# Optimization experiments

Measured on AMD Instinct MI355X. Metric: run time of the kernel, lower is better.

## Reference

```python
import jax, jax.numpy as jnp
import numpy as np

EPS_FEAT = 1.0 + 1e-4   # feature_map offset: elu(x) + 1.0 + 0.0001
EPS_DEN = 1e-6


def setup_inputs() -> dict:
    key = jax.random.key(0)
    k1, k2, k3 = jax.random.split(key, 3)
    B, L, D = 4, 4096, 1024
    x = jax.random.normal(k1, (B, L, D), dtype=jnp.float32)
    # torch Linear-style init scale ~ 1/sqrt(fan_in)
    W_qkv = jax.random.normal(k2, (D, 3 * D), dtype=jnp.float32) / np.sqrt(D)
    b_qkv = jnp.zeros((3 * D,), dtype=jnp.float32)
    W_out = jax.random.normal(k3, (D, D), dtype=jnp.float32) / np.sqrt(D)
    b_out = jnp.zeros((D,), dtype=jnp.float32)
    return {"x": x, "W_qkv": W_qkv, "b_qkv": b_qkv, "W_out": W_out, "b_out": b_out}


def _linear_attention(x, W_qkv, b_qkv, W_out, b_out, num_heads=16):
    B, L, D = x.shape
    H = num_heads
    E = D // H

    qkv = x @ W_qkv + b_qkv                       # (B, L, 3D)
    q, k, v = jnp.split(qkv, 3, axis=-1)
    q = q.reshape(B, L, H, E)
    k = k.reshape(B, L, H, E)
    v = v.reshape(B, L, H, E)

    q = jax.nn.elu(q * (E ** -0.5)) + EPS_FEAT    # scale BEFORE feature map (as in source)
    k = jax.nn.elu(k) + EPS_FEAT

    # Causal linear attention via recurrence over L; math identical to
    # cumsum of k \otimes v outer products, but never materializes (B,L,H,E,E).
    qL = jnp.moveaxis(q, 1, 0)                    # (L, B, H, E)
    kL = jnp.moveaxis(k, 1, 0)
    vL = jnp.moveaxis(v, 1, 0)

    kv0 = jnp.zeros((B, H, E, E), dtype=x.dtype)
    ks0 = jnp.zeros((B, H, E), dtype=x.dtype)

    def step(carry, qkv_t):
        kv_s, k_s = carry
        q_t, k_t, v_t = qkv_t                     # each (B, H, E)
        kv_s = kv_s + jnp.einsum('bhe,bhf->bhef', k_t, v_t)
        k_s = k_s + k_t
        num = jnp.einsum('bhe,bhef->bhf', q_t, kv_s)           # (B, H, E)
        den = jnp.einsum('bhe,bhe->bh', q_t, k_s)[..., None] + EPS_DEN
        return (kv_s, k_s), num / den

    _, out = jax.lax.scan(step, (kv0, ks0), (qL, kL, vL))       # out: (L, B, H, E)
    out = jnp.moveaxis(out, 0, 1).reshape(B, L, D)
    # dropout is identity in eval mode
    return out @ W_out + b_out


def reference(x, W_qkv, b_qkv, W_out, b_out):
    return _linear_attention(x, W_qkv, b_qkv, W_out, b_out)
```

## Files before the change

### kernel.cpp

```cpp
#include <hip/hip_runtime.h>
#include <hip/hip_bf16.h>
#include <stdint.h>

#define B_ 4
#define L_ 4096
#define D_ 1024
#define H_ 16
#define E_ 64
#define M_ (B_*L_)
#define N1_ (3*D_)
#define CHK 128
#define NC (L_/CHK)
#define BH (B_*H_)

#define EPS_FEAT 1.0001f
#define EPS_DEN 1e-6f

typedef __attribute__((ext_vector_type(4))) float f32x4;
typedef __attribute__((ext_vector_type(8))) short bf16x8;

__device__ __forceinline__ unsigned short f2bf(float x) {
    union { float f; unsigned int u; } v; v.f = x;
    unsigned int r = v.u + 0x7FFFu + ((v.u >> 16) & 1u);
    return (unsigned short)(r >> 16);
}

__device__ __forceinline__ void gload_lds16(const unsigned short* g, unsigned short* l) {
    __builtin_amdgcn_global_load_lds(
        (const __attribute__((address_space(1))) unsigned int*)(const void*)g,
        (__attribute__((address_space(3))) unsigned int*)(void*)l,
        16, 0, 0);
}


__global__ __launch_bounds__(256) void cvt_x(const float* __restrict__ x,
                                             unsigned short* __restrict__ xb) {
    int i4 = blockIdx.x * 256 + threadIdx.x;
    float4 v = ((const float4*)x)[i4];
    unsigned int lo = (unsigned int)f2bf(v.x) | ((unsigned int)f2bf(v.y) << 16);
    unsigned int hi = (unsigned int)f2bf(v.z) | ((unsigned int)f2bf(v.w) << 16);
    ((uint2*)xb)[i4] = make_uint2(lo, hi);
}

__global__ __launch_bounds__(256) void transp_w(const float* __restrict__ W,
                                                unsigned short* __restrict__ WT,
                                                int K, int N) {
    __shared__ float tile[32][33];
    int kb = blockIdx.y * 32, nb = blockIdx.x * 32;
    int tx = threadIdx.x & 31, ty = threadIdx.x >> 5;
#pragma unroll
    for (int j = 0; j < 4; ++j)
        tile[ty + 8*j][tx] = W[(size_t)(kb + ty + 8*j) * N + nb + tx];
    __syncthreads();
#pragma unroll
    for (int j = 0; j < 4; ++j) {
        int nl = ty + 8*j;
        WT[(size_t)(nb + nl) * K + kb + tx] = f2bf(tile[tx][nl]);
    }
}


template<int MODE, int KDIM, int NDIM>
__global__ __launch_bounds__(512, 2) void gemm256(
    const unsigned short* __restrict__ A,
    const unsigned short* __restrict__ BT,
    const float* __restrict__ bias,
    float* __restrict__ outF,
    unsigned short* __restrict__ qf,
    unsigned short* __restrict__ kf,
    unsigned short* __restrict__ vf)
{
    __shared__ __align__(16) unsigned short smem[65536];

    const int t = threadIdx.x, lane = t & 63, w = t >> 6;
    const int wr = w >> 2, wc = w & 3;
    const int m0 = blockIdx.y * 256, n0 = blockIdx.x * 256;
    const int lr = lane & 15, lg = lane >> 4;

    int srow[2], scol[2];
#pragma unroll
    for (int i = 0; i < 2; ++i) {
        int c = i * 512 + t;
        int row = c >> 2, s = c & 3;
        srow[i] = row;
        scol[i] = ((s ^ ((row >> 1) & 3)) << 3);
    }

    f32x4 acc[8][4] = {};

    auto stage = [&](int T) {
        unsigned short* Ab = smem + (T & 3) * 16384;
        unsigned short* Bb = Ab + 8192;
        int kt = T * 32;
#pragma unroll
        for (int i = 0; i < 2; ++i) {
            gload_lds16(A  + (size_t)(m0 + srow[i]) * KDIM + kt + scol[i], &Ab[(i*512 + t) * 8]);
            gload_lds16(BT + (size_t)(n0 + srow[i]) * KDIM + kt + scol[i], &Bb[(i*512 + t) * 8]);
        }
    };

    auto compute = [&](int T) {
        const unsigned short* Ab = smem + (T & 3) * 16384;
        const unsigned short* Bb = Ab + 8192;
        bf16x8 af[8], bfr[4];
#pragma unroll
        for (int n = 0; n < 4; ++n) {
            int row = wc * 64 + n * 16 + lr;
            bfr[n] = *(const bf16x8*)&Bb[row * 32 + ((lg ^ ((row >> 1) & 3)) << 3)];
        }
#pragma unroll
        for (int m = 0; m < 8; ++m) {
            int row = wr * 128 + m * 16 + lr;
            af[m] = *(const bf16x8*)&Ab[row * 32 + ((lg ^ ((row >> 1) & 3)) << 3)];
        }
        __builtin_amdgcn_s_setprio(1);
#pragma unroll
        for (int m = 0; m < 8; ++m)
#pragma unroll
            for (int n = 0; n < 4; ++n)
                acc[m][n] = __builtin_amdgcn_mfma_f32_16x16x32_bf16(af[m], bfr[n], acc[m][n], 0, 0, 0);
        __builtin_amdgcn_s_setprio(0);
    };

    constexpr int NT = KDIM / 32;
    stage(0); stage(1); stage(2);
    asm volatile("s_waitcnt vmcnt(8)" ::: "memory");
    __builtin_amdgcn_s_barrier();
    __builtin_amdgcn_sched_barrier(0);

    for (int T = 0; T <= NT - 4; ++T) {
        stage(T + 3);
        compute(T);
        asm volatile("s_waitcnt vmcnt(8)" ::: "memory");
        __builtin_amdgcn_s_barrier();
        __builtin_amdgcn_sched_barrier(0);
    }
    compute(NT - 3);
    asm volatile("s_waitcnt vmcnt(4)" ::: "memory");
    __builtin_amdgcn_s_barrier();
    __builtin_amdgcn_sched_barrier(0);
    compute(NT - 2);
    asm volatile("s_waitcnt vmcnt(0)" ::: "memory");
    __builtin_amdgcn_s_barrier();
    __builtin_amdgcn_sched_barrier(0);
    compute(NT - 1);
    __syncthreads();

    if (MODE == 0) {
        unsigned short* cbf = smem;
        const bool isQ = (n0 < D_), isK = (n0 >= D_ && n0 < 2*D_);
        const float scale = isQ ? 0.125f : 1.0f;
        unsigned short* buf = isQ ? qf : (isK ? kf : vf);
        const int b = m0 >> 12, l0 = m0 & 4095;
        const int h0 = (n0 & 1023) >> 6;
#pragma unroll
        for (int p = 0; p < 2; ++p) {
            if (wr == p) {
#pragma unroll
                for (int n = 0; n < 4; ++n) {
                    int cl = wc*64 + n*16 + lr;
                    float bv = bias[n0 + cl];
#pragma unroll
                    for (int m = 0; m < 8; ++m)
#pragma unroll
                        for (int q = 0; q < 4; ++q) {
                            int rl = m*16 + lg*4 + q;
                            float val = (acc[m][n][q] + bv) * scale;
                            float fv = (MODE == 0 && !isQ && !isK)
                                       ? val
                                       : ((val > 0.f ? val : __expf(val) - 1.f) + EPS_FEAT);
                            if (!isQ && !isK) fv = val;
                            cbf[rl * 264 + cl] = f2bf(fv);
                        }
                }
            }
            __syncthreads();
#pragma unroll
            for (int hh = 0; hh < 4; ++hh) {
                unsigned short* dst = buf + (((size_t)(b * H_ + h0 + hh)) * L_ + l0 + p*128) * E_;
#pragma unroll
                for (int i = 0; i < 2; ++i) {
                    int c = i*512 + t, row = c >> 3, ch = c & 7;
                    uint4 v = *(const uint4*)&cbf[row * 264 + hh*64 + ch*8];
                    *(uint4*)&dst[row * 64 + ch*8] = v;
                }
            }
            __syncthreads();
        }
    } else {
        float* cfl = (float*)smem;
#pragma unroll
        for (int p = 0; p < 4; ++p) {
            if (wr == (p >> 1)) {
                int mbase = (p & 1) * 4;
#pragma unroll
                for (int n = 0; n < 4; ++n) {
                    int cl = wc*64 + n*16 + lr;
                    float bv = bias[n0 + cl];
#pragma unroll
                    for (int mm = 0; mm < 4; ++mm)
#pragma unroll
                        for (int q = 0; q < 4; ++q) {
                            int rl = mm*16 + lg*4 + q;
                            cfl[rl * 260 + cl] = acc[mbase + mm][n][q] + bv;
                        }
                }
            }
            __syncthreads();
#pragma unroll
            for (int i = 0; i < 8; ++i) {
                int c = i*512 + t, row = c >> 6, ch = c & 63;
                float4 v = *(const float4*)&cfl[row * 260 + ch*4];
                *(float4*)&outF[(size_t)(m0 + p*64 + row) * NDIM + n0 + ch*4] = v;
            }
            __syncthreads();
        }
    }
}


__global__ __launch_bounds__(256) void chunk_kv(
    const unsigned short* __restrict__ kf, const unsigned short* __restrict__ vf,
    float* __restrict__ kvout, float* __restrict__ ksout)
{
    constexpr int LDK = 136;
    __shared__ unsigned short Kt[64 * LDK];
    __shared__ unsigned short Vt[80 * LDK];

    int t = threadIdx.x, lane = t & 63, w = t >> 6;
    int bid = blockIdx.x;
    const unsigned short* kp = kf + (size_t)bid * CHK * E_;
    const unsigned short* vp = vf + (size_t)bid * CHK * E_;

#pragma unroll
    for (int it = 0; it < 4; ++it) {
        int s = it * 256 + t;
        int rl = s >> 3, e0 = (s & 7) << 3;
        uint4 kv8 = *(const uint4*)(kp + s * 8);
        uint4 vv8 = *(const uint4*)(vp + s * 8);
        unsigned int kw[4] = {kv8.x, kv8.y, kv8.z, kv8.w};
        unsigned int vw[4] = {vv8.x, vv8.y, vv8.z, vv8.w};
#pragma unroll
        for (int jw = 0; jw < 4; ++jw) {
            Kt[(e0 + 2*jw    ) * LDK + rl] = (unsigned short)(kw[jw] & 0xFFFF);
            Kt[(e0 + 2*jw + 1) * LDK + rl] = (unsigned short)(kw[jw] >> 16);
            Vt[(e0 + 2*jw    ) * LDK + rl] = (unsigned short)(vw[jw] & 0xFFFF);
            Vt[(e0 + 2*jw + 1) * LDK + rl] = (unsigned short)(vw[jw] >> 16);
        }
    }
    if (t < 128) Vt[64 * LDK + t] = 0x3F80;
    for (int i = t; i < 15 * LDK; i += 256) Vt[65 * LDK + i] = 0;
    __syncthreads();

    int lr = lane & 15, lg = lane >> 4;
    f32x4 acc[5] = {};
#pragma unroll
    for (int ks = 0; ks < 4; ++ks) {
        bf16x8 a = *(const bf16x8*)&Kt[(w*16 + lr) * LDK + ks*32 + lg*8];
#pragma unroll
        for (int n = 0; n < 5; ++n) {
            bf16x8 b = *(const bf16x8*)&Vt[(n*16 + lr) * LDK + ks*32 + lg*8];
            acc[n] = __builtin_amdgcn_mfma_f32_16x16x32_bf16(a, b, acc[n], 0, 0, 0);
        }
    }
    float* kvo = kvout + (size_t)bid * E_ * E_;
#pragma unroll
    for (int n = 0; n < 4; ++n)
#pragma unroll
        for (int q = 0; q < 4; ++q) {
            int e = w*16 + lg*4 + q, f = n*16 + lr;
            kvo[e * 64 + f] = acc[n][q];
        }
    if (lr == 0) {
#pragma unroll
        for (int q = 0; q < 4; ++q) {
            int e = w*16 + lg*4 + q;
            ksout[(size_t)bid * 64 + e] = acc[4][q];
        }
    }
}


__global__ __launch_bounds__(256) void prefix_kv(float* __restrict__ kv, float* __restrict__ ks) {
    int bh = blockIdx.y, part = blockIdx.x, t = threadIdx.x;
    float st[4];
#pragma unroll
    for (int j = 0; j < 4; ++j) st[j] = 0.f;
    for (int c = 0; c < NC; ++c) {
        float* p = kv + ((size_t)bh * NC + c) * 4096 + part * 1024;
#pragma unroll
        for (int j = 0; j < 4; ++j) {
            float tmp = p[j * 256 + t];
            p[j * 256 + t] = st[j];
            st[j] += tmp;
        }
    }
    if (part == 0 && t < 64) {
        float s0 = 0.f;
        for (int c = 0; c < NC; ++c) {
            float* p = ks + ((size_t)bh * NC + c) * 64;
            float tmp = p[t]; p[t] = s0; s0 += tmp;
        }
    }
}


__global__ __launch_bounds__(256) void attn_out(
    const unsigned short* __restrict__ qf, const unsigned short* __restrict__ kf,
    const unsigned short* __restrict__ vf, const float* __restrict__ kvst,
    const float* __restrict__ ksst, unsigned short* __restrict__ attn)
{
    constexpr int LQ = 72;
    constexpr int LV = 136;
    constexpr int LKV = 72;
    __shared__ unsigned short Qs[128 * LQ];
    __shared__ unsigned short Ks[128 * LQ];
    __shared__ unsigned short Vt[80 * LV];
    __shared__ unsigned short KVt[80 * LKV];
    __shared__ unsigned short Ss[128 * LV];

    int t = threadIdx.x, lane = t & 63, w = t >> 6;
    int bid = blockIdx.x;
    int bh = bid >> 5, c = bid & 31;
    const unsigned short* qp = qf + (size_t)bid * CHK * E_;
    const unsigned short* kp = kf + (size_t)bid * CHK * E_;
    const unsigned short* vp = vf + (size_t)bid * CHK * E_;

#pragma unroll
    for (int it = 0; it < 4; ++it) {
        int s = it * 256 + t;
        int r = s >> 3, e0 = (s & 7) << 3;
        uint4 qv = *(const uint4*)(qp + s * 8);
        uint4 kv = *(const uint4*)(kp + s * 8);
        uint4 vv = *(const uint4*)(vp + s * 8);
        *(uint4*)&Qs[r * LQ + e0] = qv;
        *(uint4*)&Ks[r * LQ + e0] = kv;
        unsigned int vw[4] = {vv.x, vv.y, vv.z, vv.w};
#pragma unroll
        for (int jw = 0; jw < 4; ++jw) {
            Vt[(e0 + 2*jw    ) * LV + r] = (unsigned short)(vw[jw] & 0xFFFF);
            Vt[(e0 + 2*jw + 1) * LV + r] = (unsigned short)(vw[jw] >> 16);
        }
    }
    const float* kvp = kvst + (size_t)bid * 4096;
#pragma unroll
    for (int it = 0; it < 16; ++it) {
        int idx = it * 256 + t;
        int e = idx >> 6, f = idx & 63;
        KVt[f * LKV + e] = f2bf(kvp[idx]);
    }
    if (t < 64)  KVt[64 * LKV + t] = f2bf(ksst[(size_t)bid * 64 + t]);
    if (t < 128) Vt[64 * LV + t] = 0x3F80;
    for (int i = t; i < 15 * LV;  i += 256) Vt[65 * LV  + i] = 0;
    for (int i = t; i < 15 * LKV; i += 256) KVt[65 * LKV + i] = 0;
    __syncthreads();

    int lr = lane & 15, lg = lane >> 4;

#pragma unroll
    for (int m = 0; m < 2; ++m) {
        int rbase = w * 32 + m * 16;
        bf16x8 aq0 = *(const bf16x8*)&Qs[(rbase + lr) * LQ + lg*8];
        bf16x8 aq1 = *(const bf16x8*)&Qs[(rbase + lr) * LQ + 32 + lg*8];
        int jmax = 2 * w + m;
        for (int jb = 0; jb < 8; ++jb) {
            if (jb <= jmax) {
                f32x4 sacc = {};
                bf16x8 b0 = *(const bf16x8*)&Ks[(jb*16 + lr) * LQ + lg*8];
                bf16x8 b1 = *(const bf16x8*)&Ks[(jb*16 + lr) * LQ + 32 + lg*8];
                sacc = __builtin_amdgcn_mfma_f32_16x16x32_bf16(aq0, b0, sacc, 0, 0, 0);
                sacc = __builtin_amdgcn_mfma_f32_16x16x32_bf16(aq1, b1, sacc, 0, 0, 0);
#pragma unroll
                for (int q = 0; q < 4; ++q) {
                    int r = rbase + lg*4 + q;
                    int j = jb*16 + lr;
                    Ss[r * LV + j] = (j <= r) ? f2bf(sacc[q]) : (unsigned short)0;
                }
            } else {
#pragma unroll
                for (int q = 0; q < 4; ++q) {
                    int r = rbase + lg*4 + q;
                    Ss[r * LV + jb*16 + lr] = 0;
                }
            }
        }
    }

    f32x4 oacc[2][5] = {};
#pragma unroll
    for (int m = 0; m < 2; ++m) {
        int rbase = w * 32 + m * 16;
#pragma unroll
        for (int ks = 0; ks < 2; ++ks) {
            bf16x8 a = *(const bf16x8*)&Qs[(rbase + lr) * LQ + ks*32 + lg*8];
#pragma unroll
            for (int n = 0; n < 5; ++n) {
                bf16x8 b = *(const bf16x8*)&KVt[(n*16 + lr) * LKV + ks*32 + lg*8];
                oacc[m][n] = __builtin_amdgcn_mfma_f32_16x16x32_bf16(a, b, oacc[m][n], 0, 0, 0);
            }
        }
        for (int ks = 0; ks <= w; ++ks) {
            bf16x8 a = *(const bf16x8*)&Ss[(rbase + lr) * LV + ks*32 + lg*8];
#pragma unroll
            for (int n = 0; n < 5; ++n) {
                bf16x8 b = *(const bf16x8*)&Vt[(n*16 + lr) * LV + ks*32 + lg*8];
                oacc[m][n] = __builtin_amdgcn_mfma_f32_16x16x32_bf16(a, b, oacc[m][n], 0, 0, 0);
            }
        }
    }

    int b_idx = bh >> 4, h_idx = bh & 15;
#pragma unroll
    for (int m = 0; m < 2; ++m) {
        int rbase = w * 32 + m * 16;
        float den[4];
#pragma unroll
        for (int q = 0; q < 4; ++q)
            den[q] = __shfl(oacc[m][4][q], lane & 48, 64) + EPS_DEN;
#pragma unroll
        for (int n = 0; n < 4; ++n) {
#pragma unroll
            for (int q = 0; q < 4; ++q) {
                int r = rbase + lg*4 + q;
                int lpos = c * CHK + r;
                int col = n*16 + lr;
                size_t dst = ((size_t)b_idx * L_ + lpos) * D_ + h_idx * 64 + col;
                attn[dst] = f2bf(oacc[m][n][q] / den[q]);
            }
        }
    }
}


extern "C" void kernel_launch(void* const* d_in, const int* in_sizes, int n_in,
                              void* d_out, int out_size, void* d_ws, size_t ws_size,
                              hipStream_t stream)
{
    const float* x    = (const float*)d_in[0];
    const float* Wqkv = (const float*)d_in[1];
    const float* bqkv = (const float*)d_in[2];
    const float* Wout = (const float*)d_in[3];
    const float* bout = (const float*)d_in[4];
    float* out = (float*)d_out;

    char* ws = (char*)d_ws;
    size_t off = 0;
    auto alloc = [&](size_t bytes) { void* p = ws + off; off += (bytes + 255) & ~(size_t)255; return p; };
    unsigned short* xb  = (unsigned short*)alloc((size_t)M_ * D_ * 2);
    unsigned short* WqT = (unsigned short*)alloc((size_t)N1_ * D_ * 2);
    unsigned short* WoT = (unsigned short*)alloc((size_t)D_ * D_ * 2);
    unsigned short* qfb = (unsigned short*)alloc((size_t)M_ * D_ * 2);
    unsigned short* kfb = (unsigned short*)alloc((size_t)M_ * D_ * 2);
    unsigned short* vfb = (unsigned short*)alloc((size_t)M_ * D_ * 2);
    float* kvw = (float*)alloc((size_t)BH * NC * E_ * E_ * 4);
    float* ksw = (float*)alloc((size_t)BH * NC * E_ * 4);
    unsigned short* attn = xb;

    cvt_x<<<(M_ * D_ / 4) / 256, 256, 0, stream>>>(x, xb);
    transp_w<<<dim3(N1_ / 32, D_ / 32), 256, 0, stream>>>(Wqkv, WqT, D_, N1_);
    transp_w<<<dim3(D_ / 32, D_ / 32), 256, 0, stream>>>(Wout, WoT, D_, D_);

    gemm256<0, D_, N1_><<<dim3(N1_ / 256, M_ / 256), 512, 0, stream>>>(
        xb, WqT, bqkv, nullptr, qfb, kfb, vfb);

    chunk_kv<<<BH * NC, 256, 0, stream>>>(kfb, vfb, kvw, ksw);
    prefix_kv<<<dim3(4, BH), 256, 0, stream>>>(kvw, ksw);
    attn_out<<<BH * NC, 256, 0, stream>>>(qfb, kfb, vfb, kvw, ksw, attn);

    gemm256<1, D_, D_><<<dim3(D_ / 256, M_ / 256), 512, 0, stream>>>(
        attn, WoT, bout, out, nullptr, nullptr, nullptr);
}
```

Measured before the change: 287.2 us.

## Split GEMM k-step into interleaved halves, swizzle tile order, emit bf16 prefix state

The GEMM main loop now splits each k-tile into two halves. Each half issues half of the next-stage global-to-LDS loads between its LDS fragment reads and MFMA bursts, with extra barriers, to overlap memory traffic with compute more finely. Workgroup IDs are remapped with an XCD-style swizzle (bid%8 groups), meant to improve L2 locality across chiplets. The prefix-sum kernel now writes the exclusive KV/ks states as bf16 into new buffers, so attn_out reads half the bytes and skips per-element conversion; this costs extra workspace and adds more barriers inside the GEMM.

Result: no change. 282.4 us (-1.7%).

```diff
diff --git a/kernel.cpp b/kernel.cpp
--- a/kernel.cpp
+++ b/kernel.cpp
@@ -74,7 +74,12 @@
 
     const int t = threadIdx.x, lane = t & 63, w = t >> 6;
     const int wr = w >> 2, wc = w & 3;
-    const int m0 = blockIdx.y * 256, n0 = blockIdx.x * 256;
+
+    const int nwgx = NDIM / 256;
+    const int nwg = nwgx * (M_ / 256);
+    const int bid0 = blockIdx.y * nwgx + blockIdx.x;
+    const int swz = (bid0 & 7) * (nwg >> 3) + (bid0 >> 3);
+    const int m0 = (swz / nwgx) * 256, n0 = (swz % nwgx) * 256;
     const int lr = lane & 15, lg = lane >> 4;
 
     int srow[2], scol[2];
@@ -88,62 +93,83 @@
 
     f32x4 acc[8][4] = {};
 
-    auto stage = [&](int T) {
-        unsigned short* Ab = smem + (T & 3) * 16384;
-        unsigned short* Bb = Ab + 8192;
-        int kt = T * 32;
-#pragma unroll
-        for (int i = 0; i < 2; ++i) {
-            gload_lds16(A  + (size_t)(m0 + srow[i]) * KDIM + kt + scol[i], &Ab[(i*512 + t) * 8]);
-            gload_lds16(BT + (size_t)(n0 + srow[i]) * KDIM + kt + scol[i], &Bb[(i*512 + t) * 8]);
-        }
+    auto stageHalf = [&](int T, int half) {
+        unsigned short* base = smem + (T & 3) * 16384 + half * 8192;
+        const unsigned short* src = half ? BT : A;
+        const int boff = half ? n0 : m0;
+        const int kt = T * 32;
+#pragma unroll
+        for (int i = 0; i < 2; ++i)
+            gload_lds16(src + (size_t)(boff + srow[i]) * KDIM + kt + scol[i],
+                        &base[(i*512 + t) * 8]);
     };
 
-    auto compute = [&](int T) {
+    auto tile = [&](int T, bool doStage) {
         const unsigned short* Ab = smem + (T & 3) * 16384;
         const unsigned short* Bb = Ab + 8192;
-        bf16x8 af[8], bfr[4];
+        bf16x8 af[4], bfr[4];
 #pragma unroll
         for (int n = 0; n < 4; ++n) {
             int row = wc * 64 + n * 16 + lr;
             bfr[n] = *(const bf16x8*)&Bb[row * 32 + ((lg ^ ((row >> 1) & 3)) << 3)];
         }
 #pragma unroll
-        for (int m = 0; m < 8; ++m) {
+        for (int m = 0; m < 4; ++m) {
             int row = wr * 128 + m * 16 + lr;
             af[m] = *(const bf16x8*)&Ab[row * 32 + ((lg ^ ((row >> 1) & 3)) << 3)];
         }
+        if (doStage) stageHalf(T + 3, 0);
+        __builtin_amdgcn_s_barrier();
+        asm volatile("s_waitcnt lgkmcnt(0)" ::: "memory");
+        __builtin_amdgcn_sched_barrier(0);
         __builtin_amdgcn_s_setprio(1);
 #pragma unroll
-        for (int m = 0; m < 8; ++m)
+        for (int m = 0; m < 4; ++m)
 #pragma unroll
             for (int n = 0; n < 4; ++n)
                 acc[m][n] = __builtin_amdgcn_mfma_f32_16x16x32_bf16(af[m], bfr[n], acc[m][n], 0, 0, 0);
         __builtin_amdgcn_s_setprio(0);
+#pragma unroll
+        for (int m = 0; m < 4; ++m) {
+            int row = wr * 128 + (m + 4) * 16 + lr;
+            af[m] = *(const bf16x8*)&Ab[row * 32 + ((lg ^ ((row >> 1) & 3)) << 3)];
+        }
+        if (doStage) stageHalf(T + 3, 1);
+        __builtin_amdgcn_s_barrier();
+        asm volatile("s_waitcnt lgkmcnt(0)" ::: "memory");
+        __builtin_amdgcn_sched_barrier(0);
+        __builtin_amdgcn_s_setprio(1);
+#pragma unroll
+        for (int m = 0; m < 4; ++m)
+#pragma unroll
+            for (int n = 0; n < 4; ++n)
+                acc[m + 4][n] = __builtin_amdgcn_mfma_f32_16x16x32_bf16(af[m], bfr[n], acc[m + 4][n], 0, 0, 0);
+        __builtin_amdgcn_s_setprio(0);
     };
 
     constexpr int NT = KDIM / 32;
-    stage(0); stage(1); stage(2);
+    stageHalf(0,0); stageHalf(0,1);
+    stageHalf(1,0); stageHalf(1,1);
+    stageHalf(2,0); stageHalf(2,1);
     asm volatile("s_waitcnt vmcnt(8)" ::: "memory");
     __builtin_amdgcn_s_barrier();
     __builtin_amdgcn_sched_barrier(0);
 
     for (int T = 0; T <= NT - 4; ++T) {
-        stage(T + 3);
-        compute(T);
+        tile(T, true);
         asm volatile("s_waitcnt vmcnt(8)" ::: "memory");
         __builtin_amdgcn_s_barrier();
         __builtin_amdgcn_sched_barrier(0);
     }
-    compute(NT - 3);
+    tile(NT - 3, false);
     asm volatile("s_waitcnt vmcnt(4)" ::: "memory");
     __builtin_amdgcn_s_barrier();
     __builtin_amdgcn_sched_barrier(0);
-    compute(NT - 2);
+    tile(NT - 2, false);
     asm volatile("s_waitcnt vmcnt(0)" ::: "memory");
     __builtin_amdgcn_s_barrier();
     __builtin_amdgcn_sched_barrier(0);
-    compute(NT - 1);
+    tile(NT - 1, false);
     __syncthreads();
 
     if (MODE == 0) {
@@ -166,10 +192,9 @@
                         for (int q = 0; q < 4; ++q) {
                             int rl = m*16 + lg*4 + q;
                             float val = (acc[m][n][q] + bv) * scale;
-                            float fv = (MODE == 0 && !isQ && !isK)
-                                       ? val
-                                       : ((val > 0.f ? val : __expf(val) - 1.f) + EPS_FEAT);
-                            if (!isQ && !isK) fv = val;
+                            float fv = (isQ || isK)
+                                       ? ((val > 0.f ? val : __expf(val) - 1.f) + EPS_FEAT)
+                                       : val;
                             cbf[rl * 264 + cl] = f2bf(fv);
                         }
                 }
@@ -281,25 +306,30 @@
 }
 
 
-__global__ __launch_bounds__(256) void prefix_kv(float* __restrict__ kv, float* __restrict__ ks) {
+__global__ __launch_bounds__(256) void prefix_kv(
+    const float* __restrict__ kv, const float* __restrict__ ks,
+    unsigned short* __restrict__ kvb, unsigned short* __restrict__ ksb)
+{
     int bh = blockIdx.y, part = blockIdx.x, t = threadIdx.x;
     float st[4];
 #pragma unroll
     for (int j = 0; j < 4; ++j) st[j] = 0.f;
     for (int c = 0; c < NC; ++c) {
-        float* p = kv + ((size_t)bh * NC + c) * 4096 + part * 1024;
+        const float* p = kv + ((size_t)bh * NC + c) * 4096 + part * 1024;
+        unsigned short* q = kvb + ((size_t)bh * NC + c) * 4096 + part * 1024;
 #pragma unroll
         for (int j = 0; j < 4; ++j) {
             float tmp = p[j * 256 + t];
-            p[j * 256 + t] = st[j];
+            q[j * 256 + t] = f2bf(st[j]);
             st[j] += tmp;
         }
     }
     if (part == 0 && t < 64) {
         float s0 = 0.f;
         for (int c = 0; c < NC; ++c) {
-            float* p = ks + ((size_t)bh * NC + c) * 64;
-            float tmp = p[t]; p[t] = s0; s0 += tmp;
+            float tmp = ks[((size_t)bh * NC + c) * 64 + t];
+            ksb[((size_t)bh * NC + c) * 64 + t] = f2bf(s0);
+            s0 += tmp;
         }
     }
 }
@@ -307,8 +337,8 @@
 
 __global__ __launch_bounds__(256) void attn_out(
     const unsigned short* __restrict__ qf, const unsigned short* __restrict__ kf,
-    const unsigned short* __restrict__ vf, const float* __restrict__ kvst,
-    const float* __restrict__ ksst, unsigned short* __restrict__ attn)
+    const unsigned short* __restrict__ vf, const unsigned short* __restrict__ kvb,
+    const unsigned short* __restrict__ ksb, unsigned short* __restrict__ attn)
 {
     constexpr int LQ = 72;
     constexpr int LV = 136;
@@ -342,14 +372,14 @@
             Vt[(e0 + 2*jw + 1) * LV + r] = (unsigned short)(vw[jw] >> 16);
         }
     }
-    const float* kvp = kvst + (size_t)bid * 4096;
+    const unsigned short* kvp = kvb + (size_t)bid * 4096;
 #pragma unroll
     for (int it = 0; it < 16; ++it) {
         int idx = it * 256 + t;
         int e = idx >> 6, f = idx & 63;
-        KVt[f * LKV + e] = f2bf(kvp[idx]);
-    }
-    if (t < 64)  KVt[64 * LKV + t] = f2bf(ksst[(size_t)bid * 64 + t]);
+        KVt[f * LKV + e] = kvp[idx];
+    }
+    if (t < 64)  KVt[64 * LKV + t] = ksb[(size_t)bid * 64 + t];
     if (t < 128) Vt[64 * LV + t] = 0x3F80;
     for (int i = t; i < 15 * LV;  i += 256) Vt[65 * LV  + i] = 0;
     for (int i = t; i < 15 * LKV; i += 256) KVt[65 * LKV + i] = 0;
@@ -454,6 +484,8 @@
     unsigned short* vfb = (unsigned short*)alloc((size_t)M_ * D_ * 2);
     float* kvw = (float*)alloc((size_t)BH * NC * E_ * E_ * 4);
     float* ksw = (float*)alloc((size_t)BH * NC * E_ * 4);
+    unsigned short* kvb = (unsigned short*)alloc((size_t)BH * NC * E_ * E_ * 2);
+    unsigned short* ksb = (unsigned short*)alloc((size_t)BH * NC * E_ * 2);
     unsigned short* attn = xb;
 
     cvt_x<<<(M_ * D_ / 4) / 256, 256, 0, stream>>>(x, xb);
@@ -464,8 +496,8 @@
         xb, WqT, bqkv, nullptr, qfb, kfb, vfb);
 
     chunk_kv<<<BH * NC, 256, 0, stream>>>(kfb, vfb, kvw, ksw);
-    prefix_kv<<<dim3(4, BH), 256, 0, stream>>>(kvw, ksw);
-    attn_out<<<BH * NC, 256, 0, stream>>>(qfb, kfb, vfb, kvw, ksw, attn);
+    prefix_kv<<<dim3(4, BH), 256, 0, stream>>>(kvw, ksw, kvb, ksb);
+    attn_out<<<BH * NC, 256, 0, stream>>>(qfb, kfb, vfb, kvb, ksb, attn);
 
     gemm256<1, D_, D_><<<dim3(D_ / 256, M_ / 256), 512, 0, stream>>>(
         attn, WoT, bout, out, nullptr, nullptr, nullptr);
```
